# Optimization experiments

Hardware: AMD Instinct MI355X
Metric: run time of the kernel (lower is better)

Reference implementation:

```python
import jax, jax.numpy as jnp
import numpy as np
import math

N_DRUG, N_DIS, D, EMB, HEADS, STEPS = 3072, 3072, 64, 16, 4, 5
N = N_DRUG + N_DIS


def setup_inputs() -> dict:
    key = jax.random.key(0)
    ks = jax.random.split(key, 16)
    s = lambda fan: 1.0 / np.sqrt(fan)
    return {
        "graph": jax.random.uniform(ks[0], (N, N), jnp.float32),
        "drug_f": jax.random.normal(ks[1], (N_DRUG, D), jnp.float32),
        "disease_f": jax.random.normal(ks[2], (N_DIS, D), jnp.float32),
        "timesteps": jax.random.randint(ks[3], (N,), 0, STEPS, jnp.int32),
        "drug_w": jax.random.normal(ks[4], (D, D), jnp.float32) * s(D),
        "disease_w": jax.random.normal(ks[5], (D, D), jnp.float32) * s(D),
        "emb_w": jax.random.normal(ks[6], (EMB, EMB), jnp.float32) * s(EMB),
        "emb_b": jnp.zeros((EMB,), jnp.float32),
        "in_w": jax.random.normal(ks[7], (D + EMB, 256), jnp.float32) * s(D + EMB),
        "in_b": jnp.zeros((256,), jnp.float32),
        "out_w": jax.random.normal(ks[8], (256, D), jnp.float32) * s(256),
        "out_b": jnp.zeros((D,), jnp.float32),
        "wq": jax.random.normal(ks[9], (D, D), jnp.float32) * s(D),
        "bq": jnp.zeros((D,), jnp.float32),
        "wk": jax.random.normal(ks[10], (D, D), jnp.float32) * s(D),
        "bk": jnp.zeros((D,), jnp.float32),
        "wv": jax.random.normal(ks[11], (D, D), jnp.float32) * s(D),
        "bv": jnp.zeros((D,), jnp.float32),
        "wo": jax.random.normal(ks[12], (D, D), jnp.float32) * s(D),
        "bo": jnp.zeros((D,), jnp.float32),
        "fuse_w": jax.random.normal(ks[13], (2 * D, D), jnp.float32) * s(2 * D),
        "fuse_b": jnp.zeros((D,), jnp.float32),
        "ln_g": jnp.ones((D,), jnp.float32),
        "ln_b": jnp.zeros((D,), jnp.float32),
    }


def _layernorm(x, g, b, eps=1e-5):
    mu = jnp.mean(x, axis=-1, keepdims=True)
    var = jnp.var(x, axis=-1, keepdims=True)
    return (x - mu) * jax.lax.rsqrt(var + eps) * g + b


def reference(graph, drug_f, disease_f, timesteps, drug_w, disease_w,
              emb_w, emb_b, in_w, in_b, out_w, out_b,
              wq, bq, wk, bk, wv, bv, wo, bo,
              fuse_w, fuse_b, ln_g, ln_b):
    # ---- DGLLayer: per-type projection + symmetric degree-norm propagation ----
    node_f = jnp.concatenate([drug_f @ drug_w, disease_f @ disease_w], axis=0)  # [N, D]
    degs = jnp.clip(jnp.sum(graph, axis=1), 1.0, None)
    norm = jax.lax.rsqrt(degs)[:, None]  # degs^-0.5, [N, 1]
    target = (graph @ (node_f * norm)) * norm

    # ---- Denoise MLP with sinusoidal time embedding ----
    half = EMB // 2
    freqs = jnp.exp(-math.log(10000.0) * jnp.arange(half, dtype=jnp.float32) / half)
    temp = timesteps.astype(jnp.float32)[:, None] * freqs[None]  # [N, half]
    time_emb = jnp.concatenate([jnp.cos(temp), jnp.sin(temp)], axis=-1)  # [N, EMB]
    emb = time_emb @ emb_w + emb_b
    h = jnp.concatenate([target, emb], axis=-1)  # [N, D+EMB]
    h = jnp.tanh(h @ in_w + in_b)  # in-layer
    aux = h @ out_w + out_b        # final out-layer (no tanh)

    # ---- AttentionFusion: cross-attention(target -> aux) + fuse + residual LN ----
    hd = D // HEADS
    q = (target @ wq + bq).reshape(N, HEADS, hd)
    k = (aux @ wk + bk).reshape(N, HEADS, hd)
    v = (aux @ wv + bv).reshape(N, HEADS, hd)
    scores = jnp.einsum('nhd,mhd->hnm', q, k) / np.sqrt(hd)  # [H, N, N]
    attn = jax.nn.softmax(scores, axis=-1)
    attn_out = jnp.einsum('hnm,mhd->nhd', attn, v).reshape(N, D) @ wo + bo
    fused = jnp.concatenate([target, attn_out], axis=-1) @ fuse_w + fuse_b
    return _layernorm(fused + target, ln_g, ln_b)
```

## Files before the change

### kernel.cpp

```cpp
#include <hip/hip_runtime.h>
#include <cstdint>
#include <cstddef>

#define NTOT 6144
#define NDRUG 3072
#define NM (NTOT*64)
#define NSLICE 16
#define KSLICE 384
#define NKT 6

typedef __fp16 f16;
typedef __attribute__((ext_vector_type(2))) __fp16 f16x2;
typedef __attribute__((ext_vector_type(4))) __fp16 f16x4;
typedef __attribute__((ext_vector_type(8))) __fp16 f16x8;
typedef __attribute__((ext_vector_type(4))) float f32x4;

__device__ __forceinline__ f16x8 pack8(float4 a, float4 b){
  f16x2 p0 = __builtin_amdgcn_cvt_pkrtz(a.x, a.y);
  f16x2 p1 = __builtin_amdgcn_cvt_pkrtz(a.z, a.w);
  f16x2 p2 = __builtin_amdgcn_cvt_pkrtz(b.x, b.y);
  f16x2 p3 = __builtin_amdgcn_cvt_pkrtz(b.z, b.w);
  f16x4 lo = __builtin_shufflevector(p0, p1, 0, 1, 2, 3);
  f16x4 hi = __builtin_shufflevector(p2, p3, 0, 1, 2, 3);
  return __builtin_shufflevector(lo, hi, 0, 1, 2, 3, 4, 5, 6, 7);
}

__global__ __launch_bounds__(256) void k_deg(const float* __restrict__ g,
                                             const float* __restrict__ drug_f,
                                             const float* __restrict__ dis_f,
                                             const float* __restrict__ drug_w,
                                             const float* __restrict__ dis_w,
                                             float* __restrict__ norm,
                                             f16* __restrict__ nfst){
  __shared__ float sx[4][64];
  __shared__ float snf[4][64];
  int wv = threadIdx.x >> 6, j = threadIdx.x & 63;
  int row = blockIdx.x*4 + wv;
  const float4* p = (const float4*)(g + (size_t)row * NTOT);
  float s = 0.f;
  #pragma unroll
  for (int it = 0; it < 24; ++it) {
    float4 u = p[it*64 + j];
    s += (u.x + u.y) + (u.z + u.w);
  }
  #pragma unroll
  for (int off = 32; off; off >>= 1) s += __shfl_xor(s, off, 64);
  float nrm = rsqrtf(fmaxf(s, 1.0f));
  if (j == 0) norm[row] = nrm;

  const float* x; const float* W;
  if (row < NDRUG){ x = drug_f + (size_t)row*64; W = drug_w; }
  else            { x = dis_f + (size_t)(row-NDRUG)*64; W = dis_w; }
  sx[wv][j] = x[j];
  __syncthreads();
  float acc = 0.f;
  #pragma unroll 8
  for (int k = 0; k < 64; ++k) acc = fmaf(sx[wv][k], W[k*64+j], acc);
  snf[wv][j] = acc * nrm;
  __syncthreads();
  if (threadIdx.x < 64){
    int c = threadIdx.x;
    f16x4 pk = {(f16)snf[0][c], (f16)snf[1][c], (f16)snf[2][c], (f16)snf[3][c]};
    *(f16x4*)(nfst + (size_t)c*NTOT + blockIdx.x*4) = pk;
  }
}

__global__ __launch_bounds__(256) void k_gemm(const float* __restrict__ graph,
                                              const f16* __restrict__ nfst,
                                              float* __restrict__ part){
  __shared__ f16 sA[64][72];
  __shared__ f16 sB[64][72];
  const int tid = threadIdx.x;
  const int lane = tid & 63, w = tid >> 6;
  const int l15 = lane & 15, quad = lane >> 4;
  const int row0 = blockIdx.x * 64;
  const int kbase = blockIdx.y * KSLICE;
  const int sr = tid >> 2, scg = (tid & 3) * 16;

  f32x4 acc[4] = {{0.f,0.f,0.f,0.f},{0.f,0.f,0.f,0.f},
                  {0.f,0.f,0.f,0.f},{0.f,0.f,0.f,0.f}};
  float4 a0, a1, a2, a3;
  f16x8 b0, b1;
  auto LOADT = [&](int kt){
    const float4* pa = (const float4*)(graph + (size_t)(row0 + sr)*NTOT + kbase + kt*64 + scg);
    a0 = pa[0]; a1 = pa[1]; a2 = pa[2]; a3 = pa[3];
    const f16* pb = nfst + (size_t)sr*NTOT + kbase + kt*64 + scg;
    b0 = *(const f16x8*)pb; b1 = *(const f16x8*)(pb + 8);
  };
  auto WRITET = [&](){
    *(f16x8*)&sA[sr][scg]     = pack8(a0, a1);
    *(f16x8*)&sA[sr][scg + 8] = pack8(a2, a3);
    *(f16x8*)&sB[sr][scg]     = b0;
    *(f16x8*)&sB[sr][scg + 8] = b1;
  };
  LOADT(0);
  WRITET();
  __syncthreads();
  for (int kt = 0; kt < NKT; ++kt){
    if (kt + 1 < NKT) LOADT(kt + 1);
    #pragma unroll
    for (int k16 = 0; k16 < 4; ++k16){
      f16x4 af = *(const f16x4*)&sA[w*16 + l15][k16*16 + quad*4];
      #pragma unroll
      for (int nt = 0; nt < 4; ++nt){
        f16x4 bf = *(const f16x4*)&sB[nt*16 + l15][k16*16 + quad*4];
        acc[nt] = __builtin_amdgcn_mfma_f32_16x16x16f16(af, bf, acc[nt], 0, 0, 0);
      }
    }
    if (kt + 1 < NKT){
      __syncthreads();
      WRITET();
      __syncthreads();
    }
  }
  float* dst = part + (size_t)blockIdx.y * NM;
  #pragma unroll
  for (int nt = 0; nt < 4; ++nt){
    #pragma unroll
    for (int r = 0; r < 4; ++r){
      int row = row0 + w*16 + quad*4 + r;
      dst[(size_t)row*64 + nt*16 + l15] = acc[nt][r];
    }
  }
}

__global__ __launch_bounds__(256) void k_node2(const float* __restrict__ part,
                                               const float* __restrict__ norm,
                                               const int* __restrict__ ts,
                                               const float* __restrict__ emb_w,
                                               const float* __restrict__ emb_b,
                                               const float* __restrict__ in_w,
                                               const float* __restrict__ in_b,
                                               const float* __restrict__ out_w,
                                               const float* __restrict__ out_b,
                                               const float* __restrict__ wq, const float* __restrict__ bq,
                                               const float* __restrict__ wk, const float* __restrict__ bk,
                                               const float* __restrict__ wvw, const float* __restrict__ bv,
                                               float* __restrict__ target,
                                               f16* __restrict__ qh, f16* __restrict__ kh,
                                               f16* __restrict__ vt){
  __shared__ float sx[4][80];
  __shared__ float sh[4][256];
  __shared__ float sa[4][64];
  __shared__ float sv[4][64];
  int wv = threadIdx.x>>6, j = threadIdx.x&63;
  int row = blockIdx.x*4 + wv;

  float t = 0.f;
  #pragma unroll
  for (int p = 0; p < NSLICE; ++p) t += part[(size_t)p*NM + (size_t)row*64 + j];
  t *= norm[row];
  target[(size_t)row*64 + j] = t;
  sx[wv][j] = t;
  if (j < 16) {
    const float FREQ[8] = {1.0f, 0.316227766016838f, 0.1f, 0.0316227766016838f,
                           0.01f, 0.00316227766016838f, 0.001f, 0.000316227766016838f};
    float tt = (float)ts[row];
    float e = emb_b[j];
    #pragma unroll
    for (int k = 0; k < 8; ++k) {
      float a = tt * FREQ[k];
      e = fmaf(cosf(a), emb_w[k*16 + j], e);
      e = fmaf(sinf(a), emb_w[(8+k)*16 + j], e);
    }
    sx[wv][64 + j] = e;
  }
  __syncthreads();
  float a0 = in_b[4*j+0], a1 = in_b[4*j+1], a2 = in_b[4*j+2], a3 = in_b[4*j+3];
  #pragma unroll 8
  for (int k = 0; k < 80; ++k) {
    float xv = sx[wv][k];
    float4 w = *(const float4*)(in_w + k*256 + 4*j);
    a0 = fmaf(xv, w.x, a0);
    a1 = fmaf(xv, w.y, a1);
    a2 = fmaf(xv, w.z, a2);
    a3 = fmaf(xv, w.w, a3);
  }
  sh[wv][4*j+0] = tanhf(a0); sh[wv][4*j+1] = tanhf(a1);
  sh[wv][4*j+2] = tanhf(a2); sh[wv][4*j+3] = tanhf(a3);
  __syncthreads();
  float o = out_b[j];
  #pragma unroll 8
  for (int k = 0; k < 256; ++k) o = fmaf(sh[wv][k], out_w[k*64 + j], o);
  sa[wv][j] = o;
  __syncthreads();
  float q = bq[j], kk = bk[j], vv = bv[j];
  #pragma unroll 8
  for (int k = 0; k < 64; ++k) {
    float tv = sx[wv][k], av = sa[wv][k];
    q  = fmaf(tv, wq[k*64+j],  q);
    kk = fmaf(av, wk[k*64+j],  kk);
    vv = fmaf(av, wvw[k*64+j], vv);
  }
  qh[(size_t)row*64+j] = (f16)(q * 0.360673760222241f);
  kh[(size_t)row*64+j] = (f16)kk;
  sv[wv][j] = vv;
  __syncthreads();
  if (threadIdx.x < 64){
    int c = threadIdx.x;
    f16x4 pk = {(f16)sv[0][c], (f16)sv[1][c], (f16)sv[2][c], (f16)sv[3][c]};
    *(f16x4*)(vt + (size_t)c*NTOT + blockIdx.x*4) = pk;
  }
}

__global__ __launch_bounds__(256) void k_attn(const f16* __restrict__ qh,
                                              const f16* __restrict__ kh,
                                              const f16* __restrict__ vt,
                                              float* __restrict__ opart,
                                              float* __restrict__ lpart){
  __shared__ f16 sK[64][72];
  __shared__ f16 sV[64][72];
  const int tid = threadIdx.x;
  const int h = tid >> 6;
  const int lane = tid & 63;
  const int l15 = lane & 15, quad = lane >> 4;
  const int z = blockIdx.y;
  const int q0 = blockIdx.x * 64;

  f16x4 qf[4];
  #pragma unroll
  for (int qn = 0; qn < 4; ++qn)
    qf[qn] = *(const f16x4*)(qh + (size_t)(q0 + qn*16 + l15)*64 + h*16 + quad*4);

  f32x4 accOT[4] = {{0.f,0.f,0.f,0.f},{0.f,0.f,0.f,0.f},
                    {0.f,0.f,0.f,0.f},{0.f,0.f,0.f,0.f}};
  float lsum[4] = {0.f, 0.f, 0.f, 0.f};
  const int sr = tid >> 2, scg = (tid & 3) * 16;
  const int kbase = z * KSLICE;
  f16x8 k0r, k1r, v0r, v1r;
  auto LOADT = [&](int kt){
    const int k0 = kbase + kt*64;
    const f16* pk = kh + (size_t)(k0 + sr)*64 + scg;
    k0r = *(const f16x8*)pk; k1r = *(const f16x8*)(pk + 8);
    const f16* pv = vt + (size_t)sr*NTOT + k0 + scg;
    v0r = *(const f16x8*)pv; v1r = *(const f16x8*)(pv + 8);
  };
  auto WRITET = [&](){
    *(f16x8*)&sK[sr][scg]     = k0r;
    *(f16x8*)&sK[sr][scg + 8] = k1r;
    *(f16x8*)&sV[sr][scg]     = v0r;
    *(f16x8*)&sV[sr][scg + 8] = v1r;
  };
  LOADT(0);
  WRITET();
  __syncthreads();
  for (int kt = 0; kt < NKT; ++kt){
    if (kt + 1 < NKT) LOADT(kt + 1);
    #pragma unroll
    for (int km = 0; km < 4; ++km){
      f16x4 kf = *(const f16x4*)&sK[km*16 + l15][h*16 + quad*4];
      f16x4 vf = *(const f16x4*)&sV[h*16 + l15][km*16 + quad*4];
      #pragma unroll
      for (int qn = 0; qn < 4; ++qn){
        f32x4 s = __builtin_amdgcn_mfma_f32_16x16x16f16(
            kf, qf[qn], (f32x4){0.f,0.f,0.f,0.f}, 0, 0, 0);
        float p0 = exp2f(fminf(s[0], 14.4269504088896f));
        float p1 = exp2f(fminf(s[1], 14.4269504088896f));
        float p2 = exp2f(fminf(s[2], 14.4269504088896f));
        float p3 = exp2f(fminf(s[3], 14.4269504088896f));
        lsum[qn] += (p0 + p1) + (p2 + p3);
        f16x2 plo = __builtin_amdgcn_cvt_pkrtz(p0, p1);
        f16x2 phi = __builtin_amdgcn_cvt_pkrtz(p2, p3);
        f16x4 pf = __builtin_shufflevector(plo, phi, 0, 1, 2, 3);
        accOT[qn] = __builtin_amdgcn_mfma_f32_16x16x16f16(vf, pf, accOT[qn], 0, 0, 0);
      }
    }
    if (kt + 1 < NKT){
      __syncthreads();
      WRITET();
      __syncthreads();
    }
  }
  #pragma unroll
  for (int qn = 0; qn < 4; ++qn){
    lsum[qn] += __shfl_xor(lsum[qn], 16, 64);
    lsum[qn] += __shfl_xor(lsum[qn], 32, 64);
  }
  #pragma unroll
  for (int qn = 0; qn < 4; ++qn){
    const int row = q0 + qn*16 + l15;
    *(float4*)(opart + (size_t)z*NM + (size_t)row*64 + h*16 + quad*4) =
        make_float4(accOT[qn][0], accOT[qn][1], accOT[qn][2], accOT[qn][3]);
    if (quad == 0) lpart[((size_t)z*4 + h)*NTOT + row] = lsum[qn];
  }
}

__global__ __launch_bounds__(256) void k_out(const float* __restrict__ opart,
                                             const float* __restrict__ lpart,
                                             const float* __restrict__ target,
                                             const float* __restrict__ wo, const float* __restrict__ bo,
                                             const float* __restrict__ fuse_w, const float* __restrict__ fuse_b,
                                             const float* __restrict__ ln_g, const float* __restrict__ ln_b,
                                             float* __restrict__ out){
  __shared__ float st[4][64], sa[4][64], sao[4][64];
  int wv = threadIdx.x>>6, j = threadIdx.x&63;
  int row = blockIdx.x*4 + wv;
  int h = j >> 4;
  float osum = 0.f, L = 0.f;
  #pragma unroll
  for (int z = 0; z < NSLICE; ++z) {
    osum += opart[(size_t)z*NM + (size_t)row*64 + j];
    L    += lpart[((size_t)z*4 + h)*NTOT + row];
  }
  sa[wv][j] = osum / L;
  st[wv][j] = target[(size_t)row*64+j];
  __syncthreads();
  float ao = bo[j];
  #pragma unroll 8
  for (int k = 0; k < 64; ++k) ao = fmaf(sa[wv][k], wo[k*64+j], ao);
  sao[wv][j] = ao;
  __syncthreads();
  float f = fuse_b[j];
  #pragma unroll 8
  for (int k = 0; k < 64; ++k) f = fmaf(st[wv][k], fuse_w[k*64+j], f);
  #pragma unroll 8
  for (int k = 0; k < 64; ++k) f = fmaf(sao[wv][k], fuse_w[(64+k)*64+j], f);
  float x = f + st[wv][j];
  float s1 = x, s2 = x*x;
  #pragma unroll
  for (int off = 32; off; off >>= 1) { s1 += __shfl_xor(s1, off, 64); s2 += __shfl_xor(s2, off, 64); }
  float mu = s1*(1.f/64.f);
  float var = s2*(1.f/64.f) - mu*mu;
  float y = (x-mu)*rsqrtf(var + 1e-5f)*ln_g[j] + ln_b[j];
  out[(size_t)row*64 + j] = y;
}

extern "C" void kernel_launch(void* const* d_in, const int* in_sizes, int n_in,
                              void* d_out, int out_size, void* d_ws, size_t ws_size,
                              hipStream_t stream) {
  const float* graph  = (const float*)d_in[0];
  const float* drug_f = (const float*)d_in[1];
  const float* dis_f  = (const float*)d_in[2];
  const int*   ts     = (const int*)d_in[3];
  const float* drug_w = (const float*)d_in[4];
  const float* dis_w  = (const float*)d_in[5];
  const float* emb_w  = (const float*)d_in[6];
  const float* emb_b  = (const float*)d_in[7];
  const float* in_w   = (const float*)d_in[8];
  const float* in_b   = (const float*)d_in[9];
  const float* out_w  = (const float*)d_in[10];
  const float* out_b  = (const float*)d_in[11];
  const float* wq     = (const float*)d_in[12];
  const float* bq     = (const float*)d_in[13];
  const float* wk     = (const float*)d_in[14];
  const float* bk     = (const float*)d_in[15];
  const float* wvw    = (const float*)d_in[16];
  const float* bv     = (const float*)d_in[17];
  const float* wo     = (const float*)d_in[18];
  const float* bo     = (const float*)d_in[19];
  const float* fuse_w = (const float*)d_in[20];
  const float* fuse_b = (const float*)d_in[21];
  const float* ln_g   = (const float*)d_in[22];
  const float* ln_b   = (const float*)d_in[23];

  float* ws     = (float*)d_ws;
  float* norm   = ws;
  f16*   nfst   = (f16*)(ws + 8192);
  float* target = ws + 8192 + (size_t)64*NTOT/2;
  f16*   qh     = (f16*)(target + NM);
  f16*   kh     = (f16*)(target + NM + NM/2);
  f16*   vt     = (f16*)(target + NM + NM);
  float* part   = target + NM + NM + NM/2;
  float* opart  = part + (size_t)NSLICE*NM;
  float* lpart  = opart + (size_t)NSLICE*NM;

  k_deg<<<1536, 256, 0, stream>>>(graph, drug_f, dis_f, drug_w, dis_w, norm, nfst);
  k_gemm<<<dim3(96, NSLICE), 256, 0, stream>>>(graph, nfst, part);
  k_node2<<<1536, 256, 0, stream>>>(part, norm, ts, emb_w, emb_b, in_w, in_b,
                                    out_w, out_b, wq, bq, wk, bk, wvw, bv,
                                    target, qh, kh, vt);
  k_attn<<<dim3(96, NSLICE), 256, 0, stream>>>(qh, kh, vt, opart, lpart);
  k_out<<<1536, 256, 0, stream>>>(opart, lpart, target, wo, bo, fuse_w, fuse_b,
                                  ln_g, ln_b, (float*)d_out);
}
```

Before: 404.0 us.

## Fuse split-K reductions into GEMM and attention via last-block atomic counters

```diff
diff --git a/kernel.cpp b/kernel.cpp
--- a/kernel.cpp
+++ b/kernel.cpp
@@ -5,9 +5,9 @@
 #define NTOT 6144
 #define NDRUG 3072
 #define NM (NTOT*64)
-#define NSLICE 16
-#define KSLICE 384
-#define NKT 6
+#define NSLICE 8
+#define KSLICE 768
+#define NKT 12
 
 typedef __fp16 f16;
 typedef __attribute__((ext_vector_type(2))) __fp16 f16x2;
@@ -65,66 +65,8 @@
   }
 }
 
-__global__ __launch_bounds__(256) void k_gemm(const float* __restrict__ graph,
-                                              const f16* __restrict__ nfst,
-                                              float* __restrict__ part){
-  __shared__ f16 sA[64][72];
-  __shared__ f16 sB[64][72];
-  const int tid = threadIdx.x;
-  const int lane = tid & 63, w = tid >> 6;
-  const int l15 = lane & 15, quad = lane >> 4;
-  const int row0 = blockIdx.x * 64;
-  const int kbase = blockIdx.y * KSLICE;
-  const int sr = tid >> 2, scg = (tid & 3) * 16;
-
-  f32x4 acc[4] = {{0.f,0.f,0.f,0.f},{0.f,0.f,0.f,0.f},
-                  {0.f,0.f,0.f,0.f},{0.f,0.f,0.f,0.f}};
-  float4 a0, a1, a2, a3;
-  f16x8 b0, b1;
-  auto LOADT = [&](int kt){
-    const float4* pa = (const float4*)(graph + (size_t)(row0 + sr)*NTOT + kbase + kt*64 + scg);
-    a0 = pa[0]; a1 = pa[1]; a2 = pa[2]; a3 = pa[3];
-    const f16* pb = nfst + (size_t)sr*NTOT + kbase + kt*64 + scg;
-    b0 = *(const f16x8*)pb; b1 = *(const f16x8*)(pb + 8);
-  };
-  auto WRITET = [&](){
-    *(f16x8*)&sA[sr][scg]     = pack8(a0, a1);
-    *(f16x8*)&sA[sr][scg + 8] = pack8(a2, a3);
-    *(f16x8*)&sB[sr][scg]     = b0;
-    *(f16x8*)&sB[sr][scg + 8] = b1;
-  };
-  LOADT(0);
-  WRITET();
-  __syncthreads();
-  for (int kt = 0; kt < NKT; ++kt){
-    if (kt + 1 < NKT) LOADT(kt + 1);
-    #pragma unroll
-    for (int k16 = 0; k16 < 4; ++k16){
-      f16x4 af = *(const f16x4*)&sA[w*16 + l15][k16*16 + quad*4];
-      #pragma unroll
-      for (int nt = 0; nt < 4; ++nt){
-        f16x4 bf = *(const f16x4*)&sB[nt*16 + l15][k16*16 + quad*4];
-        acc[nt] = __builtin_amdgcn_mfma_f32_16x16x16f16(af, bf, acc[nt], 0, 0, 0);
-      }
-    }
-    if (kt + 1 < NKT){
-      __syncthreads();
-      WRITET();
-      __syncthreads();
-    }
-  }
-  float* dst = part + (size_t)blockIdx.y * NM;
-  #pragma unroll
-  for (int nt = 0; nt < 4; ++nt){
-    #pragma unroll
-    for (int r = 0; r < 4; ++r){
-      int row = row0 + w*16 + quad*4 + r;
-      dst[(size_t)row*64 + nt*16 + l15] = acc[nt][r];
-    }
-  }
-}
-
-__global__ __launch_bounds__(256) void k_node2(const float* __restrict__ part,
+__global__ __launch_bounds__(256) void k_gemm2(const float* __restrict__ graph,
+                                               const f16* __restrict__ nfst,
                                                const float* __restrict__ norm,
                                                const int* __restrict__ ts,
                                                const float* __restrict__ emb_w,
@@ -136,193 +78,295 @@
                                                const float* __restrict__ wq, const float* __restrict__ bq,
                                                const float* __restrict__ wk, const float* __restrict__ bk,
                                                const float* __restrict__ wvw, const float* __restrict__ bv,
+                                               float* __restrict__ part,
                                                float* __restrict__ target,
                                                f16* __restrict__ qh, f16* __restrict__ kh,
-                                               f16* __restrict__ vt){
-  __shared__ float sx[4][80];
-  __shared__ float sh[4][256];
-  __shared__ float sa[4][64];
-  __shared__ float sv[4][64];
-  int wv = threadIdx.x>>6, j = threadIdx.x&63;
-  int row = blockIdx.x*4 + wv;
-
-  float t = 0.f;
-  #pragma unroll
-  for (int p = 0; p < NSLICE; ++p) t += part[(size_t)p*NM + (size_t)row*64 + j];
-  t *= norm[row];
-  target[(size_t)row*64 + j] = t;
-  sx[wv][j] = t;
-  if (j < 16) {
-    const float FREQ[8] = {1.0f, 0.316227766016838f, 0.1f, 0.0316227766016838f,
-                           0.01f, 0.00316227766016838f, 0.001f, 0.000316227766016838f};
-    float tt = (float)ts[row];
-    float e = emb_b[j];
+                                               f16* __restrict__ vt,
+                                               unsigned* __restrict__ done){
+  __shared__ __align__(16) char smem[18432];
+  __shared__ unsigned lastf;
+  const int tid = threadIdx.x;
+  const int wv = tid >> 6, j = tid & 63;
+  const int x = blockIdx.x, z = blockIdx.y;
+
+  {
+    f16 (*sA)[72] = (f16(*)[72])smem;
+    f16 (*sB)[72] = (f16(*)[72])(smem + 9216);
+    const int lane = tid & 63, w = tid >> 6;
+    const int l15 = lane & 15, quad = lane >> 4;
+    const int row0 = x * 64;
+    const int kbase = z * KSLICE;
+    const int sr = tid >> 2, scg = (tid & 3) * 16;
+
+    f32x4 acc[4] = {{0.f,0.f,0.f,0.f},{0.f,0.f,0.f,0.f},
+                    {0.f,0.f,0.f,0.f},{0.f,0.f,0.f,0.f}};
+    float4 a0, a1, a2, a3;
+    f16x8 b0, b1;
+    auto LOADT = [&](int kt){
+      const float4* pa = (const float4*)(graph + (size_t)(row0 + sr)*NTOT + kbase + kt*64 + scg);
+      a0 = pa[0]; a1 = pa[1]; a2 = pa[2]; a3 = pa[3];
+      const f16* pb = nfst + (size_t)sr*NTOT + kbase + kt*64 + scg;
+      b0 = *(const f16x8*)pb; b1 = *(const f16x8*)(pb + 8);
+    };
+    auto WRITET = [&](){
+      *(f16x8*)&sA[sr][scg]     = pack8(a0, a1);
+      *(f16x8*)&sA[sr][scg + 8] = pack8(a2, a3);
+      *(f16x8*)&sB[sr][scg]     = b0;
+      *(f16x8*)&sB[sr][scg + 8] = b1;
+    };
+    LOADT(0);
+    WRITET();
+    __syncthreads();
+    for (int kt = 0; kt < NKT; ++kt){
+      if (kt + 1 < NKT) LOADT(kt + 1);
+      #pragma unroll
+      for (int k16 = 0; k16 < 4; ++k16){
+        f16x4 af = *(const f16x4*)&sA[w*16 + l15][k16*16 + quad*4];
+        #pragma unroll
+        for (int nt = 0; nt < 4; ++nt){
+          f16x4 bf = *(const f16x4*)&sB[nt*16 + l15][k16*16 + quad*4];
+          acc[nt] = __builtin_amdgcn_mfma_f32_16x16x16f16(af, bf, acc[nt], 0, 0, 0);
+        }
+      }
+      if (kt + 1 < NKT){
+        __syncthreads();
+        WRITET();
+        __syncthreads();
+      }
+    }
+    float* dst = part + (size_t)z * NM;
     #pragma unroll
-    for (int k = 0; k < 8; ++k) {
-      float a = tt * FREQ[k];
-      e = fmaf(cosf(a), emb_w[k*16 + j], e);
-      e = fmaf(sinf(a), emb_w[(8+k)*16 + j], e);
-    }
-    sx[wv][64 + j] = e;
-  }
-  __syncthreads();
-  float a0 = in_b[4*j+0], a1 = in_b[4*j+1], a2 = in_b[4*j+2], a3 = in_b[4*j+3];
-  #pragma unroll 8
-  for (int k = 0; k < 80; ++k) {
-    float xv = sx[wv][k];
-    float4 w = *(const float4*)(in_w + k*256 + 4*j);
-    a0 = fmaf(xv, w.x, a0);
-    a1 = fmaf(xv, w.y, a1);
-    a2 = fmaf(xv, w.z, a2);
-    a3 = fmaf(xv, w.w, a3);
-  }
-  sh[wv][4*j+0] = tanhf(a0); sh[wv][4*j+1] = tanhf(a1);
-  sh[wv][4*j+2] = tanhf(a2); sh[wv][4*j+3] = tanhf(a3);
-  __syncthreads();
-  float o = out_b[j];
-  #pragma unroll 8
-  for (int k = 0; k < 256; ++k) o = fmaf(sh[wv][k], out_w[k*64 + j], o);
-  sa[wv][j] = o;
-  __syncthreads();
-  float q = bq[j], kk = bk[j], vv = bv[j];
-  #pragma unroll 8
-  for (int k = 0; k < 64; ++k) {
-    float tv = sx[wv][k], av = sa[wv][k];
-    q  = fmaf(tv, wq[k*64+j],  q);
-    kk = fmaf(av, wk[k*64+j],  kk);
-    vv = fmaf(av, wvw[k*64+j], vv);
-  }
-  qh[(size_t)row*64+j] = (f16)(q * 0.360673760222241f);
-  kh[(size_t)row*64+j] = (f16)kk;
-  sv[wv][j] = vv;
-  __syncthreads();
-  if (threadIdx.x < 64){
-    int c = threadIdx.x;
-    f16x4 pk = {(f16)sv[0][c], (f16)sv[1][c], (f16)sv[2][c], (f16)sv[3][c]};
-    *(f16x4*)(vt + (size_t)c*NTOT + blockIdx.x*4) = pk;
+    for (int nt = 0; nt < 4; ++nt){
+      #pragma unroll
+      for (int r = 0; r < 4; ++r){
+        int row = row0 + w*16 + quad*4 + r;
+        __builtin_nontemporal_store(acc[nt][r], &dst[(size_t)row*64 + nt*16 + l15]);
+      }
+    }
+  }
+
+  __syncthreads();
+  if (tid == 0){
+    __threadfence();
+    unsigned v = __hip_atomic_fetch_add(done + x, 1u, __ATOMIC_ACQ_REL,
+                                        __HIP_MEMORY_SCOPE_AGENT);
+    lastf = (v == NSLICE - 1) ? 1u : 0u;
+    if (lastf) __threadfence();
+  }
+  __syncthreads();
+  if (!lastf) return;
+
+  {
+    float (*sx)[80]  = (float(*)[80])smem;
+    float (*sh)[256] = (float(*)[256])(smem + 1280);
+    float (*sa)[64]  = (float(*)[64])(smem + 5376);
+    float (*sv)[64]  = (float(*)[64])(smem + 6400);
+    for (int g = 0; g < 16; ++g){
+      const int bi = x*16 + g;
+      const int row = bi*4 + wv;
+      float t = 0.f;
+      #pragma unroll
+      for (int p = 0; p < NSLICE; ++p) t += part[(size_t)p*NM + (size_t)row*64 + j];
+      t *= norm[row];
+      target[(size_t)row*64 + j] = t;
+      sx[wv][j] = t;
+      if (j < 16) {
+        const float FREQ[8] = {1.0f, 0.316227766016838f, 0.1f, 0.0316227766016838f,
+                               0.01f, 0.00316227766016838f, 0.001f, 0.000316227766016838f};
+        float tt = (float)ts[row];
+        float e = emb_b[j];
+        #pragma unroll
+        for (int k = 0; k < 8; ++k) {
+          float a = tt * FREQ[k];
+          e = fmaf(cosf(a), emb_w[k*16 + j], e);
+          e = fmaf(sinf(a), emb_w[(8+k)*16 + j], e);
+        }
+        sx[wv][64 + j] = e;
+      }
+      __syncthreads();
+      float a0 = in_b[4*j+0], a1 = in_b[4*j+1], a2 = in_b[4*j+2], a3 = in_b[4*j+3];
+      #pragma unroll 8
+      for (int k = 0; k < 80; ++k) {
+        float xv = sx[wv][k];
+        float4 w = *(const float4*)(in_w + k*256 + 4*j);
+        a0 = fmaf(xv, w.x, a0);
+        a1 = fmaf(xv, w.y, a1);
+        a2 = fmaf(xv, w.z, a2);
+        a3 = fmaf(xv, w.w, a3);
+      }
+      sh[wv][4*j+0] = tanhf(a0); sh[wv][4*j+1] = tanhf(a1);
+      sh[wv][4*j+2] = tanhf(a2); sh[wv][4*j+3] = tanhf(a3);
+      __syncthreads();
+      float o = out_b[j];
+      #pragma unroll 8
+      for (int k = 0; k < 256; ++k) o = fmaf(sh[wv][k], out_w[k*64 + j], o);
+      sa[wv][j] = o;
+      __syncthreads();
+      float q = bq[j], kk = bk[j], vv = bv[j];
+      #pragma unroll 8
+      for (int k = 0; k < 64; ++k) {
+        float tv = sx[wv][k], av = sa[wv][k];
+        q  = fmaf(tv, wq[k*64+j],  q);
+        kk = fmaf(av, wk[k*64+j],  kk);
+        vv = fmaf(av, wvw[k*64+j], vv);
+      }
+      qh[(size_t)row*64+j] = (f16)(q * 0.360673760222241f);
+      kh[(size_t)row*64+j] = (f16)kk;
+      sv[wv][j] = vv;
+      __syncthreads();
+      if (tid < 64){
+        int c = tid;
+        f16x4 pk = {(f16)sv[0][c], (f16)sv[1][c], (f16)sv[2][c], (f16)sv[3][c]};
+        *(f16x4*)(vt + (size_t)c*NTOT + bi*4) = pk;
+      }
+      __syncthreads();
+    }
   }
 }
 
-__global__ __launch_bounds__(256) void k_attn(const f16* __restrict__ qh,
-                                              const f16* __restrict__ kh,
-                                              const f16* __restrict__ vt,
-                                              float* __restrict__ opart,
-                                              float* __restrict__ lpart){
-  __shared__ f16 sK[64][72];
-  __shared__ f16 sV[64][72];
+__global__ __launch_bounds__(256) void k_attn2(const f16* __restrict__ qh,
+                                               const f16* __restrict__ kh,
+                                               const f16* __restrict__ vt,
+                                               const float* __restrict__ target,
+                                               const float* __restrict__ wo, const float* __restrict__ bo,
+                                               const float* __restrict__ fuse_w, const float* __restrict__ fuse_b,
+                                               const float* __restrict__ ln_g, const float* __restrict__ ln_b,
+                                               float* __restrict__ opart,
+                                               float* __restrict__ lpart,
+                                               float* __restrict__ out,
+                                               unsigned* __restrict__ done){
+  __shared__ __align__(16) char smem[18432];
+  __shared__ unsigned lastf;
   const int tid = threadIdx.x;
-  const int h = tid >> 6;
-  const int lane = tid & 63;
-  const int l15 = lane & 15, quad = lane >> 4;
   const int z = blockIdx.y;
   const int q0 = blockIdx.x * 64;
 
-  f16x4 qf[4];
-  #pragma unroll
-  for (int qn = 0; qn < 4; ++qn)
-    qf[qn] = *(const f16x4*)(qh + (size_t)(q0 + qn*16 + l15)*64 + h*16 + quad*4);
-
-  f32x4 accOT[4] = {{0.f,0.f,0.f,0.f},{0.f,0.f,0.f,0.f},
-                    {0.f,0.f,0.f,0.f},{0.f,0.f,0.f,0.f}};
-  float lsum[4] = {0.f, 0.f, 0.f, 0.f};
-  const int sr = tid >> 2, scg = (tid & 3) * 16;
-  const int kbase = z * KSLICE;
-  f16x8 k0r, k1r, v0r, v1r;
-  auto LOADT = [&](int kt){
-    const int k0 = kbase + kt*64;
-    const f16* pk = kh + (size_t)(k0 + sr)*64 + scg;
-    k0r = *(const f16x8*)pk; k1r = *(const f16x8*)(pk + 8);
-    const f16* pv = vt + (size_t)sr*NTOT + k0 + scg;
-    v0r = *(const f16x8*)pv; v1r = *(const f16x8*)(pv + 8);
-  };
-  auto WRITET = [&](){
-    *(f16x8*)&sK[sr][scg]     = k0r;
-    *(f16x8*)&sK[sr][scg + 8] = k1r;
-    *(f16x8*)&sV[sr][scg]     = v0r;
-    *(f16x8*)&sV[sr][scg + 8] = v1r;
-  };
-  LOADT(0);
-  WRITET();
-  __syncthreads();
-  for (int kt = 0; kt < NKT; ++kt){
-    if (kt + 1 < NKT) LOADT(kt + 1);
+  {
+    f16 (*sK)[72] = (f16(*)[72])smem;
+    f16 (*sV)[72] = (f16(*)[72])(smem + 9216);
+    const int h = tid >> 6;
+    const int lane = tid & 63;
+    const int l15 = lane & 15, quad = lane >> 4;
+
+    f16x4 qf[4];
     #pragma unroll
-    for (int km = 0; km < 4; ++km){
-      f16x4 kf = *(const f16x4*)&sK[km*16 + l15][h*16 + quad*4];
-      f16x4 vf = *(const f16x4*)&sV[h*16 + l15][km*16 + quad*4];
-      #pragma unroll
-      for (int qn = 0; qn < 4; ++qn){
-        f32x4 s = __builtin_amdgcn_mfma_f32_16x16x16f16(
-            kf, qf[qn], (f32x4){0.f,0.f,0.f,0.f}, 0, 0, 0);
-        float p0 = exp2f(fminf(s[0], 14.4269504088896f));
-        float p1 = exp2f(fminf(s[1], 14.4269504088896f));
-        float p2 = exp2f(fminf(s[2], 14.4269504088896f));
-        float p3 = exp2f(fminf(s[3], 14.4269504088896f));
-        lsum[qn] += (p0 + p1) + (p2 + p3);
-        f16x2 plo = __builtin_amdgcn_cvt_pkrtz(p0, p1);
-        f16x2 phi = __builtin_amdgcn_cvt_pkrtz(p2, p3);
-        f16x4 pf = __builtin_shufflevector(plo, phi, 0, 1, 2, 3);
-        accOT[qn] = __builtin_amdgcn_mfma_f32_16x16x16f16(vf, pf, accOT[qn], 0, 0, 0);
-      }
-    }
-    if (kt + 1 < NKT){
-      __syncthreads();
-      WRITET();
-      __syncthreads();
-    }
-  }
-  #pragma unroll
-  for (int qn = 0; qn < 4; ++qn){
-    lsum[qn] += __shfl_xor(lsum[qn], 16, 64);
-    lsum[qn] += __shfl_xor(lsum[qn], 32, 64);
-  }
-  #pragma unroll
-  for (int qn = 0; qn < 4; ++qn){
-    const int row = q0 + qn*16 + l15;
-    *(float4*)(opart + (size_t)z*NM + (size_t)row*64 + h*16 + quad*4) =
-        make_float4(accOT[qn][0], accOT[qn][1], accOT[qn][2], accOT[qn][3]);
-    if (quad == 0) lpart[((size_t)z*4 + h)*NTOT + row] = lsum[qn];
-  }
-}
-
-__global__ __launch_bounds__(256) void k_out(const float* __restrict__ opart,
-                                             const float* __restrict__ lpart,
-                                             const float* __restrict__ target,
-                                             const float* __restrict__ wo, const float* __restrict__ bo,
-                                             const float* __restrict__ fuse_w, const float* __restrict__ fuse_b,
-                                             const float* __restrict__ ln_g, const float* __restrict__ ln_b,
-                                             float* __restrict__ out){
-  __shared__ float st[4][64], sa[4][64], sao[4][64];
-  int wv = threadIdx.x>>6, j = threadIdx.x&63;
-  int row = blockIdx.x*4 + wv;
-  int h = j >> 4;
-  float osum = 0.f, L = 0.f;
-  #pragma unroll
-  for (int z = 0; z < NSLICE; ++z) {
-    osum += opart[(size_t)z*NM + (size_t)row*64 + j];
-    L    += lpart[((size_t)z*4 + h)*NTOT + row];
-  }
-  sa[wv][j] = osum / L;
-  st[wv][j] = target[(size_t)row*64+j];
-  __syncthreads();
-  float ao = bo[j];
-  #pragma unroll 8
-  for (int k = 0; k < 64; ++k) ao = fmaf(sa[wv][k], wo[k*64+j], ao);
-  sao[wv][j] = ao;
-  __syncthreads();
-  float f = fuse_b[j];
-  #pragma unroll 8
-  for (int k = 0; k < 64; ++k) f = fmaf(st[wv][k], fuse_w[k*64+j], f);
-  #pragma unroll 8
-  for (int k = 0; k < 64; ++k) f = fmaf(sao[wv][k], fuse_w[(64+k)*64+j], f);
-  float x = f + st[wv][j];
-  float s1 = x, s2 = x*x;
-  #pragma unroll
-  for (int off = 32; off; off >>= 1) { s1 += __shfl_xor(s1, off, 64); s2 += __shfl_xor(s2, off, 64); }
-  float mu = s1*(1.f/64.f);
-  float var = s2*(1.f/64.f) - mu*mu;
-  float y = (x-mu)*rsqrtf(var + 1e-5f)*ln_g[j] + ln_b[j];
-  out[(size_t)row*64 + j] = y;
+    for (int qn = 0; qn < 4; ++qn)
+      qf[qn] = *(const f16x4*)(qh + (size_t)(q0 + qn*16 + l15)*64 + h*16 + quad*4);
+
+    f32x4 accOT[4] = {{0.f,0.f,0.f,0.f},{0.f,0.f,0.f,0.f},
+                      {0.f,0.f,0.f,0.f},{0.f,0.f,0.f,0.f}};
+    float lsum[4] = {0.f, 0.f, 0.f, 0.f};
+    const int sr = tid >> 2, scg = (tid & 3) * 16;
+    const int kbase = z * KSLICE;
+    f16x8 k0r, k1r, v0r, v1r;
+    auto LOADT = [&](int kt){
+      const int k0 = kbase + kt*64;
+      const f16* pk = kh + (size_t)(k0 + sr)*64 + scg;
+      k0r = *(const f16x8*)pk; k1r = *(const f16x8*)(pk + 8);
+      const f16* pv = vt + (size_t)sr*NTOT + k0 + scg;
+      v0r = *(const f16x8*)pv; v1r = *(const f16x8*)(pv + 8);
+    };
+    auto WRITET = [&](){
+      *(f16x8*)&sK[sr][scg]     = k0r;
+      *(f16x8*)&sK[sr][scg + 8] = k1r;
+      *(f16x8*)&sV[sr][scg]     = v0r;
+      *(f16x8*)&sV[sr][scg + 8] = v1r;
+    };
+    LOADT(0);
+    WRITET();
+    __syncthreads();
+    for (int kt = 0; kt < NKT; ++kt){
+      if (kt + 1 < NKT) LOADT(kt + 1);
+      #pragma unroll
+      for (int km = 0; km < 4; ++km){
+        f16x4 kf = *(const f16x4*)&sK[km*16 + l15][h*16 + quad*4];
+        f16x4 vf = *(const f16x4*)&sV[h*16 + l15][km*16 + quad*4];
+        #pragma unroll
+        for (int qn = 0; qn < 4; ++qn){
+          f32x4 s = __builtin_amdgcn_mfma_f32_16x16x16f16(
+              kf, qf[qn], (f32x4){0.f,0.f,0.f,0.f}, 0, 0, 0);
+          float p0 = exp2f(fminf(s[0], 14.4269504088896f));
+          float p1 = exp2f(fminf(s[1], 14.4269504088896f));
+          float p2 = exp2f(fminf(s[2], 14.4269504088896f));
+          float p3 = exp2f(fminf(s[3], 14.4269504088896f));
+          lsum[qn] += (p0 + p1) + (p2 + p3);
+          f16x2 plo = __builtin_amdgcn_cvt_pkrtz(p0, p1);
+          f16x2 phi = __builtin_amdgcn_cvt_pkrtz(p2, p3);
+          f16x4 pf = __builtin_shufflevector(plo, phi, 0, 1, 2, 3);
+          accOT[qn] = __builtin_amdgcn_mfma_f32_16x16x16f16(vf, pf, accOT[qn], 0, 0, 0);
+        }
+      }
+      if (kt + 1 < NKT){
+        __syncthreads();
+        WRITET();
+        __syncthreads();
+      }
+    }
+    #pragma unroll
+    for (int qn = 0; qn < 4; ++qn){
+      lsum[qn] += __shfl_xor(lsum[qn], 16, 64);
+      lsum[qn] += __shfl_xor(lsum[qn], 32, 64);
+    }
+    #pragma unroll
+    for (int qn = 0; qn < 4; ++qn){
+      const int row = q0 + qn*16 + l15;
+      f32x4 ov = {accOT[qn][0], accOT[qn][1], accOT[qn][2], accOT[qn][3]};
+      __builtin_nontemporal_store(
+          ov, (f32x4*)(opart + (size_t)z*NM + (size_t)row*64 + h*16 + quad*4));
+      if (quad == 0)
+        __builtin_nontemporal_store(lsum[qn], &lpart[((size_t)z*4 + h)*NTOT + row]);
+    }
+  }
+
+  __syncthreads();
+  if (tid == 0){
+    __threadfence();
+    unsigned v = __hip_atomic_fetch_add(done + blockIdx.x, 1u, __ATOMIC_ACQ_REL,
+                                        __HIP_MEMORY_SCOPE_AGENT);
+    lastf = (v == NSLICE - 1) ? 1u : 0u;
+    if (lastf) __threadfence();
+  }
+  __syncthreads();
+  if (!lastf) return;
+
+  {
+    float (*st)[64]  = (float(*)[64])smem;
+    float (*sa)[64]  = (float(*)[64])(smem + 1024);
+    float (*sao)[64] = (float(*)[64])(smem + 2048);
+    const int wv = tid >> 6, j = tid & 63;
+    const int h = j >> 4;
+    for (int g = 0; g < 16; ++g){
+      const int row = q0 + g*4 + wv;
+      float osum = 0.f, L = 0.f;
+      #pragma unroll
+      for (int zz = 0; zz < NSLICE; ++zz) {
+        osum += opart[(size_t)zz*NM + (size_t)row*64 + j];
+        L    += lpart[((size_t)zz*4 + h)*NTOT + row];
+      }
+      sa[wv][j] = osum / L;
+      st[wv][j] = target[(size_t)row*64+j];
+      __syncthreads();
+      float ao = bo[j];
+      #pragma unroll 8
+      for (int k = 0; k < 64; ++k) ao = fmaf(sa[wv][k], wo[k*64+j], ao);
+      sao[wv][j] = ao;
+      __syncthreads();
+      float f = fuse_b[j];
+      #pragma unroll 8
+      for (int k = 0; k < 64; ++k) f = fmaf(st[wv][k], fuse_w[k*64+j], f);
+      #pragma unroll 8
+      for (int k = 0; k < 64; ++k) f = fmaf(sao[wv][k], fuse_w[(64+k)*64+j], f);
+      float xx = f + st[wv][j];
+      float s1 = xx, s2 = xx*xx;
+      #pragma unroll
+      for (int off = 32; off; off >>= 1) { s1 += __shfl_xor(s1, off, 64); s2 += __shfl_xor(s2, off, 64); }
+      float mu = s1*(1.f/64.f);
+      float var = s2*(1.f/64.f) - mu*mu;
+      float y = (xx-mu)*rsqrtf(var + 1e-5f)*ln_g[j] + ln_b[j];
+      out[(size_t)row*64 + j] = y;
+      __syncthreads();
+    }
+  }
 }
 
 extern "C" void kernel_launch(void* const* d_in, const int* in_sizes, int n_in,
@@ -353,23 +397,28 @@
   const float* ln_g   = (const float*)d_in[22];
   const float* ln_b   = (const float*)d_in[23];
 
-  float* ws     = (float*)d_ws;
-  float* norm   = ws;
-  f16*   nfst   = (f16*)(ws + 8192);
-  float* target = ws + 8192 + (size_t)64*NTOT/2;
-  f16*   qh     = (f16*)(target + NM);
-  f16*   kh     = (f16*)(target + NM + NM/2);
-  f16*   vt     = (f16*)(target + NM + NM);
-  float* part   = target + NM + NM + NM/2;
-  float* opart  = part + (size_t)NSLICE*NM;
-  float* lpart  = opart + (size_t)NSLICE*NM;
-
+  float*    ws     = (float*)d_ws;
+  float*    norm   = ws;
+  unsigned* done_g = (unsigned*)(ws + 6656);
+  unsigned* done_a = done_g + 96;
+  f16*      nfst   = (f16*)(ws + 8192);
+  float*    target = ws + 8192 + (size_t)64*NTOT/2;
+  f16*      qh     = (f16*)(target + NM);
+  f16*      kh     = (f16*)(target + NM + NM/2);
+  f16*      vt     = (f16*)(target + NM + NM);
+  float*    part   = target + NM + NM + NM/2;
+  float*    opart  = part + (size_t)NSLICE*NM;
+  float*    lpart  = opart + (size_t)NSLICE*NM;
+
+  (void)hipMemsetAsync((void*)done_g, 0, 2*96*sizeof(unsigned), stream);
   k_deg<<<1536, 256, 0, stream>>>(graph, drug_f, dis_f, drug_w, dis_w, norm, nfst);
-  k_gemm<<<dim3(96, NSLICE), 256, 0, stream>>>(graph, nfst, part);
-  k_node2<<<1536, 256, 0, stream>>>(part, norm, ts, emb_w, emb_b, in_w, in_b,
-                                    out_w, out_b, wq, bq, wk, bk, wvw, bv,
-                                    target, qh, kh, vt);
-  k_attn<<<dim3(96, NSLICE), 256, 0, stream>>>(qh, kh, vt, opart, lpart);
-  k_out<<<1536, 256, 0, stream>>>(opart, lpart, target, wo, bo, fuse_w, fuse_b,
-                                  ln_g, ln_b, (float*)d_out);
+  k_gemm2<<<dim3(96, NSLICE), 256, 0, stream>>>(graph, nfst, norm, ts,
+                                                emb_w, emb_b, in_w, in_b,
+                                                out_w, out_b, wq, bq, wk, bk,
+                                                wvw, bv, part, target, qh, kh,
+                                                vt, done_g);
+  k_attn2<<<dim3(96, NSLICE), 256, 0, stream>>>(qh, kh, vt, target, wo, bo,
+                                                fuse_w, fuse_b, ln_g, ln_b,
+                                                opart, lpart, (float*)d_out,
+                                                done_a);
 }
```

Measured after the change: 705.7 us. 74.7% more time.

## Pre-convert graph to fp16 and stage GEMM/attention tiles via direct global-to-LDS loads

Applied to the files above, without the earlier changes.

```diff
diff --git a/kernel.cpp b/kernel.cpp
--- a/kernel.cpp
+++ b/kernel.cpp
@@ -5,9 +5,9 @@
 #define NTOT 6144
 #define NDRUG 3072
 #define NM (NTOT*64)
-#define NSLICE 16
-#define KSLICE 384
-#define NKT 6
+#define NSLICE 8
+#define KSLICE 768
+#define NKT 12
 
 typedef __fp16 f16;
 typedef __attribute__((ext_vector_type(2))) __fp16 f16x2;
@@ -15,15 +15,9 @@
 typedef __attribute__((ext_vector_type(8))) __fp16 f16x8;
 typedef __attribute__((ext_vector_type(4))) float f32x4;
 
-__device__ __forceinline__ f16x8 pack8(float4 a, float4 b){
-  f16x2 p0 = __builtin_amdgcn_cvt_pkrtz(a.x, a.y);
-  f16x2 p1 = __builtin_amdgcn_cvt_pkrtz(a.z, a.w);
-  f16x2 p2 = __builtin_amdgcn_cvt_pkrtz(b.x, b.y);
-  f16x2 p3 = __builtin_amdgcn_cvt_pkrtz(b.z, b.w);
-  f16x4 lo = __builtin_shufflevector(p0, p1, 0, 1, 2, 3);
-  f16x4 hi = __builtin_shufflevector(p2, p3, 0, 1, 2, 3);
-  return __builtin_shufflevector(lo, hi, 0, 1, 2, 3, 4, 5, 6, 7);
-}
+#define GLDS(g, l) __builtin_amdgcn_global_load_lds( \
+    (const __attribute__((address_space(1))) void*)(g), \
+    (__attribute__((address_space(3))) void*)(l), 16, 0, 0)
 
 __global__ __launch_bounds__(256) void k_deg(const float* __restrict__ g,
                                              const float* __restrict__ drug_f,
@@ -31,17 +25,21 @@
                                              const float* __restrict__ drug_w,
                                              const float* __restrict__ dis_w,
                                              float* __restrict__ norm,
+                                             f16* __restrict__ gh,
                                              f16* __restrict__ nfst){
   __shared__ float sx[4][64];
   __shared__ float snf[4][64];
   int wv = threadIdx.x >> 6, j = threadIdx.x & 63;
   int row = blockIdx.x*4 + wv;
   const float4* p = (const float4*)(g + (size_t)row * NTOT);
+  f16* ghrow = gh + (size_t)row * NTOT;
   float s = 0.f;
   #pragma unroll
   for (int it = 0; it < 24; ++it) {
     float4 u = p[it*64 + j];
     s += (u.x + u.y) + (u.z + u.w);
+    f16x4 pk = {(f16)u.x, (f16)u.y, (f16)u.z, (f16)u.w};
+    *(f16x4*)(ghrow + (size_t)(it*64 + j)*4) = pk;
   }
   #pragma unroll
   for (int off = 32; off; off >>= 1) s += __shfl_xor(s, off, 64);
@@ -65,53 +63,53 @@
   }
 }
 
-__global__ __launch_bounds__(256) void k_gemm(const float* __restrict__ graph,
+__global__ __launch_bounds__(256) void k_gemm(const f16* __restrict__ gh,
                                               const f16* __restrict__ nfst,
                                               float* __restrict__ part){
-  __shared__ f16 sA[64][72];
-  __shared__ f16 sB[64][72];
+  __shared__ __align__(16) f16 sA[2][4096];
+  __shared__ __align__(16) f16 sB[2][4096];
   const int tid = threadIdx.x;
   const int lane = tid & 63, w = tid >> 6;
   const int l15 = lane & 15, quad = lane >> 4;
   const int row0 = blockIdx.x * 64;
   const int kbase = blockIdx.y * KSLICE;
-  const int sr = tid >> 2, scg = (tid & 3) * 16;
+
+  const int srow8 = lane >> 3;
+  const int lch = (lane & 7) ^ srow8;
+
+  auto STAGE = [&](int kt, int b){
+    const int k0 = kbase + kt*64;
+    #pragma unroll
+    for (int i = 0; i < 2; ++i){
+      const int seg = w*2 + i;
+      const int row = seg*8 + srow8;
+      GLDS(gh   + (size_t)(row0 + row)*NTOT + k0 + lch*8, &sA[b][seg*512]);
+      GLDS(nfst + (size_t)row*NTOT         + k0 + lch*8, &sB[b][seg*512]);
+    }
+  };
 
   f32x4 acc[4] = {{0.f,0.f,0.f,0.f},{0.f,0.f,0.f,0.f},
                   {0.f,0.f,0.f,0.f},{0.f,0.f,0.f,0.f}};
-  float4 a0, a1, a2, a3;
-  f16x8 b0, b1;
-  auto LOADT = [&](int kt){
-    const float4* pa = (const float4*)(graph + (size_t)(row0 + sr)*NTOT + kbase + kt*64 + scg);
-    a0 = pa[0]; a1 = pa[1]; a2 = pa[2]; a3 = pa[3];
-    const f16* pb = nfst + (size_t)sr*NTOT + kbase + kt*64 + scg;
-    b0 = *(const f16x8*)pb; b1 = *(const f16x8*)(pb + 8);
-  };
-  auto WRITET = [&](){
-    *(f16x8*)&sA[sr][scg]     = pack8(a0, a1);
-    *(f16x8*)&sA[sr][scg + 8] = pack8(a2, a3);
-    *(f16x8*)&sB[sr][scg]     = b0;
-    *(f16x8*)&sB[sr][scg + 8] = b1;
-  };
-  LOADT(0);
-  WRITET();
-  __syncthreads();
+  const int r7 = l15 & 7;
+  const int q1 = quad >> 1, lo4 = (quad & 1) * 4;
+
+  STAGE(0, 0);
+  __syncthreads();
+  int cur = 0;
   for (int kt = 0; kt < NKT; ++kt){
-    if (kt + 1 < NKT) LOADT(kt + 1);
+    if (kt + 1 < NKT) STAGE(kt + 1, cur ^ 1);
     #pragma unroll
     for (int k16 = 0; k16 < 4; ++k16){
-      f16x4 af = *(const f16x4*)&sA[w*16 + l15][k16*16 + quad*4];
+      const int ch = ((2*k16 + q1) ^ r7);
+      f16x4 af = *(const f16x4*)&sA[cur][(w*16 + l15)*64 + ch*8 + lo4];
       #pragma unroll
       for (int nt = 0; nt < 4; ++nt){
-        f16x4 bf = *(const f16x4*)&sB[nt*16 + l15][k16*16 + quad*4];
+        f16x4 bf = *(const f16x4*)&sB[cur][(nt*16 + l15)*64 + ch*8 + lo4];
         acc[nt] = __builtin_amdgcn_mfma_f32_16x16x16f16(af, bf, acc[nt], 0, 0, 0);
       }
     }
-    if (kt + 1 < NKT){
-      __syncthreads();
-      WRITET();
-      __syncthreads();
-    }
+    __syncthreads();
+    cur ^= 1;
   }
   float* dst = part + (size_t)blockIdx.y * NM;
   #pragma unroll
@@ -208,8 +206,8 @@
                                               const f16* __restrict__ vt,
                                               float* __restrict__ opart,
                                               float* __restrict__ lpart){
-  __shared__ f16 sK[64][72];
-  __shared__ f16 sV[64][72];
+  __shared__ __align__(16) f16 sK[2][4096];
+  __shared__ __align__(16) f16 sV[2][4096];
   const int tid = threadIdx.x;
   const int h = tid >> 6;
   const int lane = tid & 63;
@@ -225,31 +223,34 @@
   f32x4 accOT[4] = {{0.f,0.f,0.f,0.f},{0.f,0.f,0.f,0.f},
                     {0.f,0.f,0.f,0.f},{0.f,0.f,0.f,0.f}};
   float lsum[4] = {0.f, 0.f, 0.f, 0.f};
-  const int sr = tid >> 2, scg = (tid & 3) * 16;
   const int kbase = z * KSLICE;
-  f16x8 k0r, k1r, v0r, v1r;
-  auto LOADT = [&](int kt){
+
+  const int srow8 = lane >> 3;
+  const int lch = (lane & 7) ^ srow8;
+  auto STAGE = [&](int kt, int b){
     const int k0 = kbase + kt*64;
-    const f16* pk = kh + (size_t)(k0 + sr)*64 + scg;
-    k0r = *(const f16x8*)pk; k1r = *(const f16x8*)(pk + 8);
-    const f16* pv = vt + (size_t)sr*NTOT + k0 + scg;
-    v0r = *(const f16x8*)pv; v1r = *(const f16x8*)(pv + 8);
+    #pragma unroll
+    for (int i = 0; i < 2; ++i){
+      const int seg = h*2 + i;
+      const int row = seg*8 + srow8;
+      GLDS(kh + (size_t)(k0 + row)*64 + lch*8, &sK[b][seg*512]);
+      GLDS(vt + (size_t)row*NTOT + k0 + lch*8, &sV[b][seg*512]);
+    }
   };
-  auto WRITET = [&](){
-    *(f16x8*)&sK[sr][scg]     = k0r;
-    *(f16x8*)&sK[sr][scg + 8] = k1r;
-    *(f16x8*)&sV[sr][scg]     = v0r;
-    *(f16x8*)&sV[sr][scg + 8] = v1r;
-  };
-  LOADT(0);
-  WRITET();
-  __syncthreads();
+
+  const int r7 = l15 & 7;
+  const int q1 = quad >> 1, lo4 = (quad & 1) * 4;
+  const int chK = ((2*h + q1) ^ r7);
+
+  STAGE(0, 0);
+  __syncthreads();
+  int cur = 0;
   for (int kt = 0; kt < NKT; ++kt){
-    if (kt + 1 < NKT) LOADT(kt + 1);
+    if (kt + 1 < NKT) STAGE(kt + 1, cur ^ 1);
     #pragma unroll
     for (int km = 0; km < 4; ++km){
-      f16x4 kf = *(const f16x4*)&sK[km*16 + l15][h*16 + quad*4];
-      f16x4 vf = *(const f16x4*)&sV[h*16 + l15][km*16 + quad*4];
+      f16x4 kf = *(const f16x4*)&sK[cur][(km*16 + l15)*64 + chK*8 + lo4];
+      f16x4 vf = *(const f16x4*)&sV[cur][(h*16 + l15)*64 + (((2*km + q1) ^ r7))*8 + lo4];
       #pragma unroll
       for (int qn = 0; qn < 4; ++qn){
         f32x4 s = __builtin_amdgcn_mfma_f32_16x16x16f16(
@@ -265,11 +266,8 @@
         accOT[qn] = __builtin_amdgcn_mfma_f32_16x16x16f16(vf, pf, accOT[qn], 0, 0, 0);
       }
     }
-    if (kt + 1 < NKT){
-      __syncthreads();
-      WRITET();
-      __syncthreads();
-    }
+    __syncthreads();
+    cur ^= 1;
   }
   #pragma unroll
   for (int qn = 0; qn < 4; ++qn){
@@ -355,8 +353,10 @@
 
   float* ws     = (float*)d_ws;
   float* norm   = ws;
-  f16*   nfst   = (f16*)(ws + 8192);
-  float* target = ws + 8192 + (size_t)64*NTOT/2;
+  f16*   gh     = (f16*)(ws + 8192);
+  float* base   = ws + 8192 + (size_t)NTOT*NTOT/2;
+  f16*   nfst   = (f16*)base;
+  float* target = base + (size_t)64*NTOT/2;
   f16*   qh     = (f16*)(target + NM);
   f16*   kh     = (f16*)(target + NM + NM/2);
   f16*   vt     = (f16*)(target + NM + NM);
@@ -364,8 +364,8 @@
   float* opart  = part + (size_t)NSLICE*NM;
   float* lpart  = opart + (size_t)NSLICE*NM;
 
-  k_deg<<<1536, 256, 0, stream>>>(graph, drug_f, dis_f, drug_w, dis_w, norm, nfst);
-  k_gemm<<<dim3(96, NSLICE), 256, 0, stream>>>(graph, nfst, part);
+  k_deg<<<1536, 256, 0, stream>>>(graph, drug_f, dis_f, drug_w, dis_w, norm, gh, nfst);
+  k_gemm<<<dim3(96, NSLICE), 256, 0, stream>>>(gh, nfst, part);
   k_node2<<<1536, 256, 0, stream>>>(part, norm, ts, emb_w, emb_b, in_w, in_b,
                                     out_w, out_b, wq, bq, wk, bk, wvw, bv,
                                     target, qh, kh, vt);
```

Result: slower. 412.1 us (+2.0%).
